# Optimization experiments

Hardware: AMD Instinct MI355X
Metric: run time of the kernel (lower is better)

The kernel has to match this reference:

```python
import jax, jax.numpy as jnp
import numpy as np

B, C, H, W = 4, 96, 64, 64
D_STATE, D_CONV, EXPAND = 16, 4, 2
D_INNER = EXPAND * C          # 192
DT_RANK = (C + 15) // 16      # 6
BN_EPS = 1e-5


def setup_inputs() -> dict:
    key = jax.random.key(0)
    ks = jax.random.split(key, 10)
    s = 0.02
    return {
        "x": jax.random.normal(ks[0], (B, C, H, W), jnp.float32),
        # Mamba block params (mamba_ssm layout, no bias on in/out proj)
        "in_proj_w": jax.random.normal(ks[1], (2 * D_INNER, C), jnp.float32) * s,
        "conv1d_w": jax.random.normal(ks[2], (D_INNER, 1, D_CONV), jnp.float32) * s,  # depthwise
        "conv1d_b": jnp.zeros((D_INNER,), jnp.float32),
        "x_proj_w": jax.random.normal(ks[3], (DT_RANK + 2 * D_STATE, D_INNER), jnp.float32) * s,
        "dt_proj_w": jax.random.normal(ks[4], (D_INNER, DT_RANK), jnp.float32) * s,
        "dt_proj_b": jax.random.normal(ks[5], (D_INNER,), jnp.float32) * s,
        "A_log": jnp.log(jnp.tile(jnp.arange(1, D_STATE + 1, dtype=jnp.float32), (D_INNER, 1))),
        "D": jnp.ones((D_INNER,), jnp.float32),
        "out_proj_w": jax.random.normal(ks[6], (C, D_INNER), jnp.float32) * s,
        # trailing ConvBNReLU6 params
        "conv2d_w": jax.random.normal(ks[7], (C, C, 3, 3), jnp.float32) * s,
        "bn_gamma": jnp.ones((C,), jnp.float32),
        "bn_beta": jnp.zeros((C,), jnp.float32),
        "bn_mean": jnp.zeros((C,), jnp.float32),
        "bn_var": jnp.ones((C,), jnp.float32),
    }


def _forward(x, in_proj_w, conv1d_w, conv1d_b, x_proj_w, dt_proj_w, dt_proj_b,
             A_log, D, out_proj_w, conv2d_w, bn_gamma, bn_beta, bn_mean, bn_var):
    b, c, h, w = x.shape
    L = h * w
    seq = x.reshape(b, c, L).transpose(0, 2, 1)              # [B, L, C] tokens
    xz = seq @ in_proj_w.T                                    # [B, L, 2*D_INNER]
    xi, z = jnp.split(xz, 2, axis=-1)

    # depthwise causal conv1d + SiLU
    xi_c = jax.lax.conv_general_dilated(
        xi.transpose(0, 2, 1), conv1d_w, (1,), [(D_CONV - 1, 0)],
        dimension_numbers=("NCH", "OIH", "NCH"), feature_group_count=D_INNER)
    xi = jax.nn.silu((xi_c + conv1d_b[None, :, None]).transpose(0, 2, 1))  # [B, L, D_INNER]

    # input-dependent dt, B, C
    x_dbl = xi @ x_proj_w.T                                   # [B, L, DT_RANK + 2*D_STATE]
    dt, Bm, Cm = jnp.split(x_dbl, [DT_RANK, DT_RANK + D_STATE], axis=-1)
    dt = jax.nn.softplus(dt @ dt_proj_w.T + dt_proj_b)        # [B, L, D_INNER]

    # discretize: dA = exp(dt*A), dBx = dt*B*x
    A = -jnp.exp(A_log)                                       # [D_INNER, D_STATE]
    dA = jnp.exp(dt[..., None] * A)                           # [B, L, D_INNER, D_STATE]
    dBx = dt[..., None] * Bm[:, :, None, :] * xi[..., None]   # [B, L, D_INNER, D_STATE]

    def step(hst, inputs):
        dA_t, dBx_t, C_t = inputs
        hst = dA_t * hst + dBx_t                              # [B, D_INNER, D_STATE]
        y_t = jnp.einsum("bds,bs->bd", hst, C_t)
        return hst, y_t

    h0 = jnp.zeros((b, D_INNER, D_STATE), xi.dtype)
    _, ys = jax.lax.scan(step, h0,
                         (dA.transpose(1, 0, 2, 3), dBx.transpose(1, 0, 2, 3), Cm.transpose(1, 0, 2)))
    y = ys.transpose(1, 0, 2)                                 # [B, L, D_INNER]
    y = (y + xi * D) * jax.nn.silu(z)                         # skip D + gate
    out = y @ out_proj_w.T                                    # [B, L, C]
    xm = out.transpose(0, 2, 1).reshape(b, c, h, w)

    # ConvBNReLU: 3x3 conv (pad 1, no bias) -> BN (inference) -> ReLU6
    xo = jax.lax.conv_general_dilated(xm, conv2d_w, (1, 1), [(1, 1), (1, 1)],
                                      dimension_numbers=("NCHW", "OIHW", "NCHW"))
    inv = bn_gamma / jnp.sqrt(bn_var + BN_EPS)
    xo = xo * inv[None, :, None, None] + (bn_beta - bn_mean * inv)[None, :, None, None]
    return jnp.clip(xo, 0.0, 6.0)


def reference(x, in_proj_w, conv1d_w, conv1d_b, x_proj_w, dt_proj_w, dt_proj_b,
              A_log, D, out_proj_w, conv2d_w, bn_gamma, bn_beta, bn_mean, bn_var):
    return _forward(x, in_proj_w, conv1d_w, conv1d_b, x_proj_w, dt_proj_w, dt_proj_b,
                    A_log, D, out_proj_w, conv2d_w, bn_gamma, bn_beta, bn_mean, bn_var)
```

## Files before the change

kernel.cpp:

```cpp
#include <hip/hip_runtime.h>
#include <math.h>

#define LQ 4096
#define DI 192
#define DS 16
#define NCHUNK 64

__device__ __forceinline__ float siluf_(float v) { return v / (1.f + __expf(-v)); }
__device__ __forceinline__ float softplusf_(float v) { return v > 20.f ? v : log1pf(__expf(v)); }

template <int CTRL>
__device__ __forceinline__ float dpp_add16_(float x) {
    int y = __builtin_amdgcn_update_dpp(0, __float_as_int(x), CTRL, 0xf, 0xf, true);
    return x + __int_as_float(y);
}
template <int CTRL>
__device__ __forceinline__ float dpp_shift_(float x) {
    int y = __builtin_amdgcn_update_dpp(0, __float_as_int(x), CTRL, 0xf, 0xf, true);
    return __int_as_float(y);
}
__device__ __forceinline__ void async_g2l16_(const float* g, float* l) {
    __builtin_amdgcn_global_load_lds(
        (const __attribute__((address_space(1))) void*)g,
        (__attribute__((address_space(3))) void*)l, 16, 0, 0);
}

__global__ __launch_bounds__(256) void k1_inproj(const float* __restrict__ x,
    const float* __restrict__ w, const float* __restrict__ cw,
    const float* __restrict__ cb, float* __restrict__ xi, float* __restrict__ z)
{
    const int l0 = blockIdx.x * 64;
    const int n0 = blockIdx.y * 64;
    const int b  = blockIdx.z;
    __shared__ float xs[96 * 64];
    __shared__ float wsT[96 * 68];
    const int tid = threadIdx.x;
    for (int i = tid; i < 96 * 16; i += 256) {
        int c = i >> 4, lq = i & 15;
        *(float4*)&xs[c * 64 + lq * 4] =
            *(const float4*)&x[(b * 96 + c) * LQ + l0 + lq * 4];
    }
    for (int i = tid; i < 64 * 24; i += 256) {
        int n = i / 24, cq = i - n * 24;
        float4 v = *(const float4*)&w[(n0 + n) * 96 + cq * 4];
        wsT[(cq * 4 + 0) * 68 + n] = v.x;
        wsT[(cq * 4 + 1) * 68 + n] = v.y;
        wsT[(cq * 4 + 2) * 68 + n] = v.z;
        wsT[(cq * 4 + 3) * 68 + n] = v.w;
    }
    __syncthreads();
    const int tx = tid & 15;
    const int ty = tid >> 4;
    float acc[4][4];
#pragma unroll
    for (int i = 0; i < 4; ++i)
#pragma unroll
        for (int j = 0; j < 4; ++j) acc[i][j] = 0.f;
    for (int k = 0; k < 96; ++k) {
        float4 a  = *(const float4*)&xs[k * 64 + ty * 4];
        float4 bb = *(const float4*)&wsT[k * 68 + tx * 4];
        float av[4] = {a.x, a.y, a.z, a.w};
        float bv[4] = {bb.x, bb.y, bb.z, bb.w};
#pragma unroll
        for (int i = 0; i < 4; ++i)
#pragma unroll
            for (int j = 0; j < 4; ++j) acc[i][j] += av[i] * bv[j];
    }
    if (n0 >= DI) {
#pragma unroll
        for (int i = 0; i < 4; ++i) {
            int l = l0 + ty * 4 + i;
            float4 v = make_float4(acc[i][0], acc[i][1], acc[i][2], acc[i][3]);
            *(float4*)&z[(b * LQ + l) * DI + (n0 - DI) + tx * 4] = v;
        }
        return;
    }
    __syncthreads();
    float* sxz = xs;
#pragma unroll
    for (int i = 0; i < 4; ++i) {
        int r = 3 + ty * 4 + i;
        *(float4*)&sxz[r * 64 + tx * 4] =
            make_float4(acc[i][0], acc[i][1], acc[i][2], acc[i][3]);
    }
    if (tid < 192) {
        int lh = tid >> 6;
        int nn = tid & 63;
        float a = 0.f;
        if (l0 > 0) {
            const float* xc = x + (size_t)b * 96 * LQ + (l0 - 3 + lh);
            for (int c = 0; c < 96; ++c)
                a += xc[c * LQ] * wsT[c * 68 + nn];
        }
        sxz[lh * 64 + nn] = a;
    }
    __syncthreads();
    {
        const int nn = tid & 63;
        const int lg = tid >> 6;
        const int d  = n0 + nn;
        float4 wv = *(const float4*)&cw[d * 4];
        float bias = cb[d];
#pragma unroll 4
        for (int p = 0; p < 16; ++p) {
            int l = lg + p * 4;
            float a = bias;
            a += wv.x * sxz[(l + 0) * 64 + nn];
            a += wv.y * sxz[(l + 1) * 64 + nn];
            a += wv.z * sxz[(l + 2) * 64 + nn];
            a += wv.w * sxz[(l + 3) * 64 + nn];
            xi[(b * LQ + l0 + l) * DI + d] = siluf_(a);
        }
    }
}

__global__ __launch_bounds__(512) void k3_xdbl(const float* __restrict__ xi,
    const float* __restrict__ xw, float* __restrict__ xdbl)
{
    const int l0 = blockIdx.x * 64;
    const int b  = blockIdx.y;
    __shared__ float sxiT[96 * 68];
    __shared__ float swx[38 * 196];
    const int tid = threadIdx.x;
    for (int i = tid; i < 38 * 48; i += 512) {
        int n = i / 48, kq = i - n * 48;
        *(float4*)&swx[n * 196 + kq * 4] = *(const float4*)&xw[n * 192 + kq * 4];
    }
    const int lq = tid & 15, ng = tid >> 4;
    float acc[2][4];
#pragma unroll
    for (int p = 0; p < 2; ++p)
#pragma unroll
        for (int i = 0; i < 4; ++i) acc[p][i] = 0.f;
    for (int half = 0; half < 2; ++half) {
        __syncthreads();
        for (int i = tid; i < 64 * 24; i += 512) {
            int l = i / 24, kq = i - l * 24;
            float4 v = *(const float4*)&xi[(b * LQ + l0 + l) * DI + half * 96 + kq * 4];
            sxiT[(kq * 4 + 0) * 68 + l] = v.x;
            sxiT[(kq * 4 + 1) * 68 + l] = v.y;
            sxiT[(kq * 4 + 2) * 68 + l] = v.z;
            sxiT[(kq * 4 + 3) * 68 + l] = v.w;
        }
        __syncthreads();
#pragma unroll
        for (int pass = 0; pass < 2; ++pass) {
            int n = pass * 32 + ng;
            if (n >= 38) continue;
            for (int k = 0; k < 96; ++k) {
                float4 a = *(const float4*)&sxiT[k * 68 + lq * 4];
                float bv = swx[n * 196 + half * 96 + k];
                acc[pass][0] += a.x * bv;
                acc[pass][1] += a.y * bv;
                acc[pass][2] += a.z * bv;
                acc[pass][3] += a.w * bv;
            }
        }
    }
#pragma unroll
    for (int pass = 0; pass < 2; ++pass) {
        int n = pass * 32 + ng;
        if (n >= 38) continue;
#pragma unroll
        for (int i = 0; i < 4; ++i)
            xdbl[(b * LQ + l0 + lq * 4 + i) * 38 + n] = acc[pass][i];
    }
}

__global__ __launch_bounds__(256) void k4_scanA(
    const float* __restrict__ xdbl, const float* __restrict__ xi,
    const float* __restrict__ dtw, const float* __restrict__ dtb,
    const float* __restrict__ alog,
    float* __restrict__ cA, float* __restrict__ cB)
{
    const int ch = blockIdx.x, g = blockIdx.y, b = blockIdx.z;
    const int t0 = ch * 64, d0 = g * 16;
    __shared__ float sxd[64 * 40];
    __shared__ float sdt[1024], sxi[1024];
    __shared__ float sdtw[96], sdtb[16];
    const int tid = threadIdx.x;
    for (int i = tid; i < 64 * 38; i += 256) {
        int t = i / 38, cc = i - t * 38;
        sxd[t * 40 + cc] = xdbl[(b * LQ + t0 + t) * 38 + cc];
    }
    for (int i = tid; i < 1024; i += 256) {
        int t = i >> 4, j = i & 15;
        sxi[i] = xi[(b * LQ + t0 + t) * DI + d0 + j];
    }
    if (tid < 96) sdtw[tid] = dtw[d0 * 6 + tid];
    if (tid < 16) sdtb[tid] = dtb[d0 + tid];
    __syncthreads();
    for (int i = tid; i < 1024; i += 256) {
        int t = i >> 4, dl = i & 15;
        float acc = sdtb[dl];
#pragma unroll
        for (int r = 0; r < 6; ++r) acc += sxd[t * 40 + r] * sdtw[dl * 6 + r];
        sdt[i] = softplusf_(acc);
    }
    __syncthreads();
    const int s = tid & 15, dl = tid >> 4;
    const float Ads = -__expf(alog[(d0 + dl) * DS + s]);
    float a = 1.f, hb = 0.f;
#pragma unroll 4
    for (int t = 0; t < 64; ++t) {
        float dtv = sdt[t * 16 + dl];
        float dA = __expf(dtv * Ads);
        float dbx = dtv * sxd[t * 40 + 6 + s] * sxi[t * 16 + dl];
        a *= dA;
        hb = dA * hb + dbx;
    }
    int o = ((b * NCHUNK + ch) * DI + d0 + dl) * DS + s;
    cA[o] = a;
    cB[o] = hb;
}

__global__ __launch_bounds__(256) void k5_combine(const float* __restrict__ cA,
    const float* __restrict__ cB, float* __restrict__ hinit)
{
    int gid = blockIdx.x * 256 + threadIdx.x;
    int b = gid / 3072;
    int rem = gid - b * 3072;
    int base = b * (NCHUNK * 3072) + rem;
    float h = 0.f;
#pragma unroll 8
    for (int c = 0; c < NCHUNK; ++c) {
        int o = base + c * 3072;
        hinit[o] = h;
        h = cA[o] * h + cB[o];
    }
}

__global__ __launch_bounds__(256) void k6_scanC(
    const float* __restrict__ xdbl, const float* __restrict__ xi,
    const float* __restrict__ z, const float* __restrict__ dtw,
    const float* __restrict__ dtb, const float* __restrict__ alog,
    const float* __restrict__ Dp, const float* __restrict__ hinit,
    float* __restrict__ yg)
{
    const int ch = blockIdx.x, g = blockIdx.y, b = blockIdx.z;
    const int t0 = ch * 64, d0 = g * 16;
    __shared__ float sxd[64 * 40];
    __shared__ float sdt[1024], sxi[1024], szs[1024], sy[1024];
    __shared__ float sdtw[96], sdtb[16];
    const int tid = threadIdx.x;
    for (int i = tid; i < 64 * 38; i += 256) {
        int t = i / 38, cc = i - t * 38;
        sxd[t * 40 + cc] = xdbl[(b * LQ + t0 + t) * 38 + cc];
    }
    for (int i = tid; i < 1024; i += 256) {
        int t = i >> 4, j = i & 15;
        int row = b * LQ + t0 + t;
        sxi[i] = xi[row * DI + d0 + j];
        szs[i] = z[row * DI + d0 + j];
    }
    if (tid < 96) sdtw[tid] = dtw[d0 * 6 + tid];
    if (tid < 16) sdtb[tid] = dtb[d0 + tid];
    __syncthreads();
    for (int i = tid; i < 1024; i += 256) {
        int t = i >> 4, dl = i & 15;
        float acc = sdtb[dl];
#pragma unroll
        for (int r = 0; r < 6; ++r) acc += sxd[t * 40 + r] * sdtw[dl * 6 + r];
        sdt[i] = softplusf_(acc);
    }
    __syncthreads();
    const int s = tid & 15, dl = tid >> 4;
    const float Ads = -__expf(alog[(d0 + dl) * DS + s]);
    float h = hinit[((b * NCHUNK + ch) * DI + d0 + dl) * DS + s];
    for (int t = 0; t < 64; ++t) {
        float dtv = sdt[t * 16 + dl];
        float dA = __expf(dtv * Ads);
        h = dA * h + dtv * sxd[t * 40 + 6 + s] * sxi[t * 16 + dl];
        float p = h * sxd[t * 40 + 22 + s];
        p = dpp_add16_<0x128>(p);
        p = dpp_add16_<0x124>(p);
        p = dpp_add16_<0x122>(p);
        p = dpp_add16_<0x121>(p);
        if (s == 0) sy[t * 16 + dl] = p;
    }
    __syncthreads();
    for (int i = tid; i < 1024; i += 256) {
        int t = i >> 4, j = i & 15;
        float gate = siluf_(szs[i]);
        yg[(b * LQ + t0 + t) * DI + d0 + j] = (sy[i] + sxi[i] * Dp[d0 + j]) * gate;
    }
}

__global__ __launch_bounds__(256) void k7_outproj(const float* __restrict__ yg,
    const float* __restrict__ wo, float* __restrict__ xm)
{
    const int l0 = blockIdx.x * 64;
    const int n0 = blockIdx.y * 32;
    const int b  = blockIdx.z;
    __shared__ float syT[96 * 68];
    __shared__ float wtT[192 * 36];
    const int tid = threadIdx.x;
    for (int i = tid; i < 32 * 48; i += 256) {
        int n = i / 48, kq = i - n * 48;
        float4 v = *(const float4*)&wo[(n0 + n) * DI + kq * 4];
        wtT[(kq * 4 + 0) * 36 + n] = v.x;
        wtT[(kq * 4 + 1) * 36 + n] = v.y;
        wtT[(kq * 4 + 2) * 36 + n] = v.z;
        wtT[(kq * 4 + 3) * 36 + n] = v.w;
    }
    const int tx = tid & 15;
    const int ty = tid >> 4;
    float acc[2][4];
#pragma unroll
    for (int j = 0; j < 2; ++j)
#pragma unroll
        for (int i = 0; i < 4; ++i) acc[j][i] = 0.f;
    for (int half = 0; half < 2; ++half) {
        __syncthreads();
        for (int i = tid; i < 64 * 24; i += 256) {
            int l = i / 24, kq = i - l * 24;
            float4 v = *(const float4*)&yg[(b * LQ + l0 + l) * DI + half * 96 + kq * 4];
            syT[(kq * 4 + 0) * 68 + l] = v.x;
            syT[(kq * 4 + 1) * 68 + l] = v.y;
            syT[(kq * 4 + 2) * 68 + l] = v.z;
            syT[(kq * 4 + 3) * 68 + l] = v.w;
        }
        __syncthreads();
        for (int k = 0; k < 96; ++k) {
            float4 a = *(const float4*)&syT[k * 68 + tx * 4];
            int kk = half * 96 + k;
            float b0 = wtT[kk * 36 + ty * 2 + 0];
            float b1 = wtT[kk * 36 + ty * 2 + 1];
            acc[0][0] += a.x * b0; acc[0][1] += a.y * b0;
            acc[0][2] += a.z * b0; acc[0][3] += a.w * b0;
            acc[1][0] += a.x * b1; acc[1][1] += a.y * b1;
            acc[1][2] += a.z * b1; acc[1][3] += a.w * b1;
        }
    }
#pragma unroll
    for (int j = 0; j < 2; ++j) {
        float4 v = make_float4(acc[j][0], acc[j][1], acc[j][2], acc[j][3]);
        *(float4*)&xm[(b * 96 + n0 + ty * 2 + j) * LQ + l0 + tx * 4] = v;
    }
}

#define K8_INQ 384
__global__ __launch_bounds__(256) void k8_conv3(const float* __restrict__ xm,
    const float* __restrict__ w2, const float* __restrict__ bng,
    const float* __restrict__ bnb, const float* __restrict__ bnm,
    const float* __restrict__ bnv, float* __restrict__ out)
{
    const int flat = blockIdx.x;
    const int xcd  = flat & 7;
    const int k    = flat >> 3;
    const int cog  = k % 12;
    const int ybh  = k / 12;
    const int yb   = ybh * 8 + xcd;
    const int y0   = (yb >> 2) * 4;
    const int b    = yb & 3;
    const int co0  = cog * 8;

    __shared__ float sin2[2][1536];
    const int tid = threadIdx.x;
    const int sx = tid & 15;
    const int sy = (tid >> 4) & 3;
    const int cq = tid >> 6;

    int in_goff[2];
    bool in_ok[2];
#pragma unroll
    for (int j = 0; j < 2; ++j) {
        int i = tid + j * 256;
        int ci  = i / 96;
        int rem = i - ci * 96;
        int row = rem >> 4;
        int qx  = rem & 15;
        int gy  = y0 + row - 1;
        bool ok = (i < K8_INQ) && gy >= 0 && gy < 64;
        in_ok[j]  = ok;
        in_goff[j] = ok ? (ci * 4096 + gy * 64 + qx * 4) : 0;
    }

    const float* xb = xm + (size_t)b * 96 * 4096;
    const float* wbu = w2 + (size_t)__builtin_amdgcn_readfirstlane(co0 + cq * 2) * 864;
    const float4 zero4 = make_float4(0.f, 0.f, 0.f, 0.f);

#pragma unroll
    for (int bu = 0; bu < 2; ++bu) {
        if (!in_ok[0]) *(float4*)&sin2[bu][tid * 4] = zero4;
        if (tid < 128 && !in_ok[1]) *(float4*)&sin2[bu][(256 + tid) * 4] = zero4;
    }

    {
        if (in_ok[0]) async_g2l16_(xb + in_goff[0], &sin2[0][cq * 256]);
        if (tid < 128 && in_ok[1]) async_g2l16_(xb + in_goff[1], &sin2[0][1024 + cq * 256]);
    }
    __syncthreads();

    float acc[2][4];
#pragma unroll
    for (int c = 0; c < 2; ++c)
#pragma unroll
        for (int x = 0; x < 4; ++x) acc[c][x] = 0.f;

#pragma clang loop unroll(disable)
    for (int ch = 0; ch < 24; ++ch) {
        if (ch < 23) {
            const int nb = (ch + 1) & 1;
            const float* gx = xb + (ch + 1) * 16384;
            if (in_ok[0]) async_g2l16_(gx + in_goff[0], &sin2[nb][cq * 256]);
            if (tid < 128 && in_ok[1]) async_g2l16_(gx + in_goff[1], &sin2[nb][1024 + cq * 256]);
        }

        const float* sc = sin2[ch & 1];
#pragma unroll
        for (int cii = 0; cii < 4; ++cii) {
            float wA[9], wB[9];
#pragma unroll
            for (int t = 0; t < 9; ++t) {
                wA[t] = wbu[ch * 36 + cii * 9 + t];
                wB[t] = wbu[864 + ch * 36 + cii * 9 + t];
            }
            float w6[3][6];
#pragma unroll
            for (int r = 0; r < 3; ++r) {
                float4 v = *(const float4*)&sc[(cii * 6 + sy + r) * 64 + sx * 4];
                w6[r][0] = dpp_shift_<0x111>(v.w);
                w6[r][1] = v.x; w6[r][2] = v.y; w6[r][3] = v.z; w6[r][4] = v.w;
                w6[r][5] = dpp_shift_<0x101>(v.x);
            }
#pragma unroll
            for (int ky = 0; ky < 3; ++ky) {
#pragma unroll
                for (int kx = 0; kx < 3; ++kx) {
                    float wa = wA[ky * 3 + kx];
                    float wb = wB[ky * 3 + kx];
#pragma unroll
                    for (int x = 0; x < 4; ++x) {
                        float pv = w6[ky][x + kx];
                        acc[0][x] = fmaf(pv, wa, acc[0][x]);
                        acc[1][x] = fmaf(pv, wb, acc[1][x]);
                    }
                }
            }
        }

        __syncthreads();
    }

    const int yy = y0 + sy;
#pragma unroll
    for (int j = 0; j < 2; ++j) {
        const int cc = co0 + cq * 2 + j;
        float inv = bng[cc] / sqrtf(bnv[cc] + 1e-5f);
        float add = bnb[cc] - bnm[cc] * inv;
        float4 o;
        o.x = fminf(fmaxf(acc[j][0] * inv + add, 0.f), 6.f);
        o.y = fminf(fmaxf(acc[j][1] * inv + add, 0.f), 6.f);
        o.z = fminf(fmaxf(acc[j][2] * inv + add, 0.f), 6.f);
        o.w = fminf(fmaxf(acc[j][3] * inv + add, 0.f), 6.f);
        *(float4*)&out[((size_t)(b * 96 + cc) * 64 + yy) * 64 + sx * 4] = o;
    }
}

extern "C" void kernel_launch(void* const* d_in, const int* in_sizes, int n_in,
                              void* d_out, int out_size, void* d_ws, size_t ws_size,
                              hipStream_t stream) {
    (void)in_sizes; (void)n_in; (void)out_size; (void)ws_size;
    const float* x    = (const float*)d_in[0];
    const float* w_in = (const float*)d_in[1];
    const float* cw   = (const float*)d_in[2];
    const float* cb   = (const float*)d_in[3];
    const float* xw   = (const float*)d_in[4];
    const float* dtw  = (const float*)d_in[5];
    const float* dtb  = (const float*)d_in[6];
    const float* alog = (const float*)d_in[7];
    const float* Dp   = (const float*)d_in[8];
    const float* wo   = (const float*)d_in[9];
    const float* w2   = (const float*)d_in[10];
    const float* bng  = (const float*)d_in[11];
    const float* bnb  = (const float*)d_in[12];
    const float* bnm  = (const float*)d_in[13];
    const float* bnv  = (const float*)d_in[14];

    float* ws = (float*)d_ws;
    float* yg     = ws;
    float* z      = ws + 3145728;
    float* xi     = ws + 6291456;
    float* xdbl   = ws + 9437184;
    float* cA     = ws + 10059776;
    float* cB     = ws + 10846208;
    float* hinit  = ws + 11632640;
    float* xm     = ws + 12419072;

    dim3 blk(256);
    k1_inproj<<<dim3(64, 6, 4), blk, 0, stream>>>(x, w_in, cw, cb, xi, z);
    k3_xdbl<<<dim3(64, 4), dim3(512), 0, stream>>>(xi, xw, xdbl);
    k4_scanA<<<dim3(NCHUNK, 12, 4), blk, 0, stream>>>(xdbl, xi, dtw, dtb, alog, cA, cB);
    k5_combine<<<dim3(48), blk, 0, stream>>>(cA, cB, hinit);
    k6_scanC<<<dim3(NCHUNK, 12, 4), blk, 0, stream>>>(xdbl, xi, z, dtw, dtb, alog, Dp, hinit, yg);
    k7_outproj<<<dim3(64, 3, 4), blk, 0, stream>>>(yg, wo, xm);
    k8_conv3<<<dim3(768), blk, 0, stream>>>(xm, w2, bng, bnb, bnm, bnv, (float*)d_out);
}
```

Before: 267.9 us.

## Split conv3x3 input channels in two and compute four output channels per thread

The 3x3 conv kernel now splits the 96 input channels into two halves (split-K) and has each thread accumulate four output channels instead of two. Each block covers 16 output channels over 48 input channels, which halves the serial channel loop and reuses each loaded input pixel across more FMAs. Partial sums go to a scratch buffer (the reused yg region), and a new reduction kernel adds the two halves and applies BN and ReLU6. The cost is an extra kernel launch, a write and re-read of two full-size partial tensors, and more registers per thread.

```diff
diff --git a/kernel.cpp b/kernel.cpp
--- a/kernel.cpp
+++ b/kernel.cpp
@@ -341,19 +341,19 @@
 
 #define K8_INQ 384
 __global__ __launch_bounds__(256) void k8_conv3(const float* __restrict__ xm,
-    const float* __restrict__ w2, const float* __restrict__ bng,
-    const float* __restrict__ bnb, const float* __restrict__ bnm,
-    const float* __restrict__ bnv, float* __restrict__ out)
+    const float* __restrict__ w2, float* __restrict__ pbuf)
 {
     const int flat = blockIdx.x;
     const int xcd  = flat & 7;
-    const int k    = flat >> 3;
-    const int cog  = k % 12;
-    const int ybh  = k / 12;
-    const int yb   = ybh * 8 + xcd;
-    const int y0   = (yb >> 2) * 4;
-    const int b    = yb & 3;
-    const int co0  = cog * 8;
+    const int kk   = flat >> 3;
+    const int cog  = kk % 6;
+    const int th   = kk / 6;
+    const int tile = th * 8 + xcd;
+    const int ks   = tile & 1;
+    const int yt   = (tile >> 1) & 15;
+    const int b    = tile >> 5;
+    const int y0   = yt * 4;
+    const int co0  = cog * 16;
 
     __shared__ float sin2[2][1536];
     const int tid = threadIdx.x;
@@ -376,8 +376,9 @@
         in_goff[j] = ok ? (ci * 4096 + gy * 64 + qx * 4) : 0;
     }
 
-    const float* xb = xm + (size_t)b * 96 * 4096;
-    const float* wbu = w2 + (size_t)__builtin_amdgcn_readfirstlane(co0 + cq * 2) * 864;
+    const float* xb = xm + (size_t)b * 96 * 4096 + (size_t)ks * 48 * 4096;
+    const float* wbu = w2 + (size_t)__builtin_amdgcn_readfirstlane(co0 + cq * 4) * 864
+                          + ks * 432;
     const float4 zero4 = make_float4(0.f, 0.f, 0.f, 0.f);
 
 #pragma unroll
@@ -392,15 +393,15 @@
     }
     __syncthreads();
 
-    float acc[2][4];
-#pragma unroll
-    for (int c = 0; c < 2; ++c)
+    float acc[4][4];
+#pragma unroll
+    for (int c = 0; c < 4; ++c)
 #pragma unroll
         for (int x = 0; x < 4; ++x) acc[c][x] = 0.f;
 
 #pragma clang loop unroll(disable)
-    for (int ch = 0; ch < 24; ++ch) {
-        if (ch < 23) {
+    for (int ch = 0; ch < 12; ++ch) {
+        if (ch < 11) {
             const int nb = (ch + 1) & 1;
             const float* gx = xb + (ch + 1) * 16384;
             if (in_ok[0]) async_g2l16_(gx + in_goff[0], &sin2[nb][cq * 256]);
@@ -410,12 +411,12 @@
         const float* sc = sin2[ch & 1];
 #pragma unroll
         for (int cii = 0; cii < 4; ++cii) {
-            float wA[9], wB[9];
-#pragma unroll
-            for (int t = 0; t < 9; ++t) {
-                wA[t] = wbu[ch * 36 + cii * 9 + t];
-                wB[t] = wbu[864 + ch * 36 + cii * 9 + t];
-            }
+            float wt[4][9];
+#pragma unroll
+            for (int c = 0; c < 4; ++c)
+#pragma unroll
+                for (int t = 0; t < 9; ++t)
+                    wt[c][t] = wbu[c * 864 + ch * 36 + cii * 9 + t];
             float w6[3][6];
 #pragma unroll
             for (int r = 0; r < 3; ++r) {
@@ -428,13 +429,13 @@
             for (int ky = 0; ky < 3; ++ky) {
 #pragma unroll
                 for (int kx = 0; kx < 3; ++kx) {
-                    float wa = wA[ky * 3 + kx];
-                    float wb = wB[ky * 3 + kx];
 #pragma unroll
                     for (int x = 0; x < 4; ++x) {
                         float pv = w6[ky][x + kx];
-                        acc[0][x] = fmaf(pv, wa, acc[0][x]);
-                        acc[1][x] = fmaf(pv, wb, acc[1][x]);
+                        acc[0][x] = fmaf(pv, wt[0][ky * 3 + kx], acc[0][x]);
+                        acc[1][x] = fmaf(pv, wt[1][ky * 3 + kx], acc[1][x]);
+                        acc[2][x] = fmaf(pv, wt[2][ky * 3 + kx], acc[2][x]);
+                        acc[3][x] = fmaf(pv, wt[3][ky * 3 + kx], acc[3][x]);
                     }
                 }
             }
@@ -444,18 +445,34 @@
     }
 
     const int yy = y0 + sy;
-#pragma unroll
-    for (int j = 0; j < 2; ++j) {
-        const int cc = co0 + cq * 2 + j;
-        float inv = bng[cc] / sqrtf(bnv[cc] + 1e-5f);
-        float add = bnb[cc] - bnm[cc] * inv;
-        float4 o;
-        o.x = fminf(fmaxf(acc[j][0] * inv + add, 0.f), 6.f);
-        o.y = fminf(fmaxf(acc[j][1] * inv + add, 0.f), 6.f);
-        o.z = fminf(fmaxf(acc[j][2] * inv + add, 0.f), 6.f);
-        o.w = fminf(fmaxf(acc[j][3] * inv + add, 0.f), 6.f);
-        *(float4*)&out[((size_t)(b * 96 + cc) * 64 + yy) * 64 + sx * 4] = o;
-    }
+    float* pb = pbuf + (size_t)ks * 1572864;
+#pragma unroll
+    for (int c = 0; c < 4; ++c) {
+        const int cc = co0 + cq * 4 + c;
+        float4 o = make_float4(acc[c][0], acc[c][1], acc[c][2], acc[c][3]);
+        *(float4*)&pb[((size_t)(b * 96 + cc) * 64 + yy) * 64 + sx * 4] = o;
+    }
+}
+
+__global__ __launch_bounds__(256) void k9_reduce(const float* __restrict__ pbuf,
+    const float* __restrict__ bng, const float* __restrict__ bnb,
+    const float* __restrict__ bnm, const float* __restrict__ bnv,
+    float* __restrict__ out)
+{
+    const int q = blockIdx.x * 256 + threadIdx.x;
+    const int idx = q * 4;
+    const int c = (idx >> 12) % 96;
+    float4 s  = *(const float4*)&pbuf[idx];
+    float4 s1 = *(const float4*)&pbuf[idx + 1572864];
+    s.x += s1.x; s.y += s1.y; s.z += s1.z; s.w += s1.w;
+    float inv = bng[c] / sqrtf(bnv[c] + 1e-5f);
+    float add = bnb[c] - bnm[c] * inv;
+    float4 o;
+    o.x = fminf(fmaxf(s.x * inv + add, 0.f), 6.f);
+    o.y = fminf(fmaxf(s.y * inv + add, 0.f), 6.f);
+    o.z = fminf(fmaxf(s.z * inv + add, 0.f), 6.f);
+    o.w = fminf(fmaxf(s.w * inv + add, 0.f), 6.f);
+    *(float4*)&out[idx] = o;
 }
 
 extern "C" void kernel_launch(void* const* d_in, const int* in_sizes, int n_in,
@@ -487,6 +504,7 @@
     float* cB     = ws + 10846208;
     float* hinit  = ws + 11632640;
     float* xm     = ws + 12419072;
+    float* pbuf   = yg;
 
     dim3 blk(256);
     k1_inproj<<<dim3(64, 6, 4), blk, 0, stream>>>(x, w_in, cw, cb, xi, z);
@@ -495,5 +513,6 @@
     k5_combine<<<dim3(48), blk, 0, stream>>>(cA, cB, hinit);
     k6_scanC<<<dim3(NCHUNK, 12, 4), blk, 0, stream>>>(xdbl, xi, z, dtw, dtb, alog, Dp, hinit, yg);
     k7_outproj<<<dim3(64, 3, 4), blk, 0, stream>>>(yg, wo, xm);
-    k8_conv3<<<dim3(768), blk, 0, stream>>>(xm, w2, bng, bnb, bnm, bnv, (float*)d_out);
-}
+    k8_conv3<<<dim3(768), blk, 0, stream>>>(xm, w2, pbuf);
+    k9_reduce<<<dim3(1536), blk, 0, stream>>>(pbuf, bng, bnb, bnm, bnv, (float*)d_out);
+}
```

New measurement: 258.7 us. -3.4%, faster.
